# Performance work log

Measured on AMD Instinct MI355X. Metric: run time of the kernel, lower is better.

The kernel has to match this reference:

```python
import jax, jax.numpy as jnp
import numpy as np

N = 10000      # nodes
E = 160000     # directed edges (script symmetrizes; random here)
IN = 512       # input feature dim
H = 512        # hidden dim
OUT = 16       # classes


def setup_inputs() -> dict:
    key = jax.random.key(0)
    ks = jax.random.split(key, 8)
    x = jax.random.normal(ks[0], (N, IN), dtype=jnp.float32)
    edge_index = jax.random.randint(ks[1], (2, E), 0, N, dtype=jnp.int64)

    def glorot(k, shape):
        lim = np.sqrt(6.0 / (shape[0] + shape[1])).astype(np.float32)
        return jax.random.uniform(k, shape, dtype=jnp.float32, minval=-lim, maxval=lim)

    W1 = glorot(ks[2], (IN, H));  b1 = jnp.zeros((H,), jnp.float32)
    W2 = glorot(ks[3], (H, H));   b2 = jnp.zeros((H,), jnp.float32)
    Wl = glorot(ks[4], (H, OUT)); bl = jnp.zeros((OUT,), jnp.float32)
    return {"x": x, "edge_index": edge_index,
            "W1": W1, "b1": b1, "W2": W2, "b2": b2, "Wl": Wl, "bl": bl}


def gcn_conv(x, edge_index, W, b):
    """PyG GCNConv: D^{-1/2}(A+I)D^{-1/2} X W + b, unit edge weights."""
    n = x.shape[0]
    src, dst = edge_index[0], edge_index[1]
    h = x @ W                                   # [N, H] transform first (in<=out path)
    # degree with self-loops (all edge weights = 1)
    deg = jnp.zeros((n,), h.dtype).at[dst].add(1.0) + 1.0
    dinv = jax.lax.rsqrt(deg)                   # deg >= 1, no inf handling needed
    norm = dinv[src] * dinv[dst]                # [E]
    msgs = norm[:, None] * h[src]               # [E, H] gather + scale
    agg = jax.ops.segment_sum(msgs, dst, num_segments=n)
    agg = agg + (dinv * dinv)[:, None] * h      # self-loop contribution
    return agg + b


def reference(x, edge_index, W1, b1, W2, b2, Wl, bl):
    h = jax.nn.relu(gcn_conv(x, edge_index, W1, b1))
    # dropout is identity at inference
    h = jax.nn.relu(gcn_conv(h, edge_index, W2, b2))
    return h @ Wl + bl                          # [N, OUT] logits
```

## Files before the change

### kernel.cpp

```cpp
#include <hip/hip_runtime.h>
#include <stdint.h>

#define NF 512
#define OUT_F 16
#define PAD_DEG 128
#define GBM 64
#define GBN 128
#define GBK 32
#define NCHUNK 4

typedef __attribute__((ext_vector_type(8))) short short8v;
typedef __attribute__((ext_vector_type(4))) float f32x4;

#define GLOAD_LDS16(g, l) \
  __builtin_amdgcn_global_load_lds((const __attribute__((address_space(1))) unsigned int*)(g), \
                                   (__attribute__((address_space(3))) unsigned int*)(l), 16, 0, 0)


__device__ __forceinline__ void split2(float x, short& h, short& l) {
    unsigned u = __builtin_bit_cast(unsigned, x);
    unsigned hb = (u + 0x7fffu + ((u >> 16) & 1u)) & 0xffff0000u;
    h = (short)(hb >> 16);
    float r = x - __builtin_bit_cast(float, hb);
    unsigned v = __builtin_bit_cast(unsigned, r);
    unsigned lb = (v + 0x7fffu + ((v >> 16) & 1u)) & 0xffff0000u;
    l = (short)(lb >> 16);
}

__device__ __forceinline__ unsigned short bf16r(float x) {
    unsigned u = __builtin_bit_cast(unsigned, x);
    return (unsigned short)((u + 0x7fffu + ((u >> 16) & 1u)) >> 16);
}


__global__ void edge_prep_kernel(const int* __restrict__ src, const int* __restrict__ dst,
                                 int* __restrict__ counts, int* __restrict__ src_pad, int E) {
    int e = blockIdx.x * blockDim.x + threadIdx.x;
    if (e < E) {
        int d = dst[e];
        int slot = atomicAdd(&counts[d], 1);
        if (slot < PAD_DEG) src_pad[(size_t)d * PAD_DEG + slot] = src[e];
    }
}


__global__ __launch_bounds__(256) void convert_w_kernel(
    const float* __restrict__ W1, const float* __restrict__ W2,
    short* __restrict__ hi1, short* __restrict__ lo1,
    short* __restrict__ hi2, short* __restrict__ lo2) {
    __shared__ float tile[64][65];
    int id = blockIdx.x;
    const float* W;  short *WH, *WL;
    if (id < 64) { W = W1; WH = hi1; WL = lo1; }
    else         { W = W2; WH = hi2; WL = lo2; id -= 64; }
    int k0 = (id & 7) * 64, n0 = (id >> 3) * 64;
    int tr = threadIdx.x >> 4;
    int tc4 = (threadIdx.x & 15) * 4;
#pragma unroll
    for (int i = 0; i < 4; ++i) {
        int r = tr + i * 16;
        float4 v = *(const float4*)(W + (size_t)(k0 + r) * NF + n0 + tc4);
        tile[r][tc4 + 0] = v.x; tile[r][tc4 + 1] = v.y;
        tile[r][tc4 + 2] = v.z; tile[r][tc4 + 3] = v.w;
    }
    __syncthreads();
#pragma unroll
    for (int i = 0; i < 4; ++i) {
        int n = tr + i * 16;
        short h[4], l[4];
#pragma unroll
        for (int j = 0; j < 4; ++j) split2(tile[tc4 + j][n], h[j], l[j]);
        size_t off = (size_t)(n0 + n) * NF + k0 + tc4;
        *(short4*)(WH + off) = make_short4(h[0], h[1], h[2], h[3]);
        *(short4*)(WL + off) = make_short4(l[0], l[1], l[2], l[3]);
    }
}


__global__ __launch_bounds__(256) void convert_x_kernel(
    const float* __restrict__ x, short* __restrict__ xhi, short* __restrict__ xlo,
    int Nreal, int Mp) {
    int idx = blockIdx.x * 256 + threadIdx.x;
    int row = idx >> 7;
    int c4 = (idx & 127) * 4;
    if (row >= Mp) return;
    float4 v = make_float4(0.f, 0.f, 0.f, 0.f);
    if (row < Nreal) v = *(const float4*)(x + (size_t)row * NF + c4);
    short h[4], l[4];
    split2(v.x, h[0], l[0]); split2(v.y, h[1], l[1]);
    split2(v.z, h[2], l[2]); split2(v.w, h[3], l[3]);
    size_t off = (size_t)row * NF + c4;
    *(short4*)(xhi + off) = make_short4(h[0], h[1], h[2], h[3]);
    *(short4*)(xlo + off) = make_short4(l[0], l[1], l[2], l[3]);
}


__global__ __launch_bounds__(256) void gemm_mfma_kernel(
    const short* __restrict__ Ahi, const short* __restrict__ Alo,
    const short* __restrict__ BhiT, const short* __restrict__ BloT,
    const int* __restrict__ counts, unsigned short* __restrict__ Cb) {
    __shared__ short lds[2 * GBM * GBK + 2 * GBN * GBK];
    short* As_hi = lds;
    short* As_lo = lds + GBM * GBK;
    short* Bs_hi = lds + 2 * GBM * GBK;
    short* Bs_lo = lds + 2 * GBM * GBK + GBN * GBK;

    int t = threadIdx.x;
    int w = t >> 6, lane = t & 63, l15 = lane & 15, q = lane >> 4;
    int m0 = (blockIdx.x >> 2) * GBM;
    int n0 = (blockIdx.x & 3) * GBN;
    int wr = w >> 1, wc = w & 1;

    int gr = lane >> 2;
    int gk = (lane & 3) * 8;
    const short* Ahi_g = Ahi + (size_t)(m0 + w * 16 + gr) * NF + gk;
    const short* Alo_g = Alo + (size_t)(m0 + w * 16 + gr) * NF + gk;
    const short* Bhi_g0 = BhiT + (size_t)(n0 + w * 16 + gr) * NF + gk;
    const short* Bhi_g1 = BhiT + (size_t)(n0 + (w + 4) * 16 + gr) * NF + gk;
    const short* Blo_g0 = BloT + (size_t)(n0 + w * 16 + gr) * NF + gk;
    const short* Blo_g1 = BloT + (size_t)(n0 + (w + 4) * 16 + gr) * NF + gk;
    short* As_hi_d = As_hi + w * 16 * GBK;
    short* As_lo_d = As_lo + w * 16 * GBK;
    short* Bs_hi_d0 = Bs_hi + w * 16 * GBK;
    short* Bs_hi_d1 = Bs_hi + (w + 4) * 16 * GBK;
    short* Bs_lo_d0 = Bs_lo + w * 16 * GBK;
    short* Bs_lo_d1 = Bs_lo + (w + 4) * 16 * GBK;

    f32x4 acc[2][4] = {};

    for (int k0 = 0; k0 < NF; k0 += GBK) {
        GLOAD_LDS16(Ahi_g + k0, As_hi_d);
        GLOAD_LDS16(Alo_g + k0, As_lo_d);
        GLOAD_LDS16(Bhi_g0 + k0, Bs_hi_d0);
        GLOAD_LDS16(Bhi_g1 + k0, Bs_hi_d1);
        GLOAD_LDS16(Blo_g0 + k0, Bs_lo_d0);
        GLOAD_LDS16(Blo_g1 + k0, Bs_lo_d1);
        __syncthreads();

        short8v ahi[2], alo[2], bhi[4], blo[4];
#pragma unroll
        for (int r = 0; r < 2; ++r) {
            int off = (wr * 32 + r * 16 + l15) * GBK + q * 8;
            ahi[r] = *(const short8v*)(As_hi + off);
            alo[r] = *(const short8v*)(As_lo + off);
        }
#pragma unroll
        for (int c = 0; c < 4; ++c) {
            int off = (wc * 64 + c * 16 + l15) * GBK + q * 8;
            bhi[c] = *(const short8v*)(Bs_hi + off);
            blo[c] = *(const short8v*)(Bs_lo + off);
        }
#pragma unroll
        for (int r = 0; r < 2; ++r)
#pragma unroll
            for (int c = 0; c < 4; ++c) {
                acc[r][c] = __builtin_amdgcn_mfma_f32_16x16x32_bf16(ahi[r], bhi[c], acc[r][c], 0, 0, 0);
                acc[r][c] = __builtin_amdgcn_mfma_f32_16x16x32_bf16(ahi[r], blo[c], acc[r][c], 0, 0, 0);
                acc[r][c] = __builtin_amdgcn_mfma_f32_16x16x32_bf16(alo[r], bhi[c], acc[r][c], 0, 0, 0);
            }
        __syncthreads();
    }

#pragma unroll
    for (int r = 0; r < 2; ++r)
#pragma unroll
        for (int i = 0; i < 4; ++i) {
            int row = m0 + wr * 32 + r * 16 + q * 4 + i;
            float dv = rsqrtf((float)counts[row] + 1.0f);
#pragma unroll
            for (int c = 0; c < 4; ++c) {
                int col = n0 + wc * 64 + c * 16 + l15;
                Cb[(size_t)row * NF + col] = bf16r(acc[r][c][i] * dv);
            }
        }
}


__global__ __launch_bounds__(256) void agg_kernel(
    const unsigned short* __restrict__ hb, const int* __restrict__ counts,
    const int* __restrict__ src_pad, const float* __restrict__ bias,
    short* __restrict__ out_hi, short* __restrict__ out_lo,
    float* __restrict__ out32, int Mreal, int split_out) {
    int chunk = blockIdx.x & (NCHUNK - 1);
    int node = (blockIdx.x >> 2) * 4 + (threadIdx.x >> 6);
    int lane = threadIdx.x & 63;
    int g = lane >> 4;
    int j = lane & 15;
    int f8 = chunk * 128 + j * 8;
    size_t obase = (size_t)node * NF + f8;

    if (node >= Mreal) {
        if (g == 0) {
            if (split_out) {
                short8v z = {0, 0, 0, 0, 0, 0, 0, 0};
                *(short8v*)(out_hi + obase) = z;
                *(short8v*)(out_lo + obase) = z;
            } else {
                *(float4*)(out32 + obase) = make_float4(0.f, 0.f, 0.f, 0.f);
                *(float4*)(out32 + obase + 4) = make_float4(0.f, 0.f, 0.f, 0.f);
            }
        }
        return;
    }

    int cntr = counts[node];
    int cnt = cntr < PAD_DEG ? cntr : PAD_DEG;
    const int* sp = src_pad + (size_t)node * PAD_DEG;

    float acc[8] = {};
    for (int e = 0; e < cnt; e += 16) {
        int4 s4 = *(const int4*)(sp + e + g * 4);
        int base = e + g * 4;
        int sidx[4] = {s4.x, s4.y, s4.z, s4.w};
#pragma unroll
        for (int tq = 0; tq < 4; ++tq) {
            bool ok = (base + tq) < cnt;
            int srow = ok ? sidx[tq] : node;
            float m = ok ? 1.f : 0.f;
            uint4 pv = *(const uint4*)(hb + (size_t)srow * NF + f8);
            acc[0] = fmaf(m, __builtin_bit_cast(float, pv.x << 16), acc[0]);
            acc[1] = fmaf(m, __builtin_bit_cast(float, pv.x & 0xffff0000u), acc[1]);
            acc[2] = fmaf(m, __builtin_bit_cast(float, pv.y << 16), acc[2]);
            acc[3] = fmaf(m, __builtin_bit_cast(float, pv.y & 0xffff0000u), acc[3]);
            acc[4] = fmaf(m, __builtin_bit_cast(float, pv.z << 16), acc[4]);
            acc[5] = fmaf(m, __builtin_bit_cast(float, pv.z & 0xffff0000u), acc[5]);
            acc[6] = fmaf(m, __builtin_bit_cast(float, pv.w << 16), acc[6]);
            acc[7] = fmaf(m, __builtin_bit_cast(float, pv.w & 0xffff0000u), acc[7]);
        }
    }

#pragma unroll
    for (int k = 0; k < 8; ++k) {
        acc[k] += __shfl_xor(acc[k], 16);
        acc[k] += __shfl_xor(acc[k], 32);
    }

    if (g != 0) return;

    uint4 sv = *(const uint4*)(hb + obase);
    float self[8];
    self[0] = __builtin_bit_cast(float, sv.x << 16);
    self[1] = __builtin_bit_cast(float, sv.x & 0xffff0000u);
    self[2] = __builtin_bit_cast(float, sv.y << 16);
    self[3] = __builtin_bit_cast(float, sv.y & 0xffff0000u);
    self[4] = __builtin_bit_cast(float, sv.z << 16);
    self[5] = __builtin_bit_cast(float, sv.z & 0xffff0000u);
    self[6] = __builtin_bit_cast(float, sv.w << 16);
    self[7] = __builtin_bit_cast(float, sv.w & 0xffff0000u);

    float dv = rsqrtf((float)cntr + 1.0f);
    float o[8];
#pragma unroll
    for (int k = 0; k < 8; ++k)
        o[k] = fmaxf(fmaf(dv, acc[k] + self[k], bias[f8 + k]), 0.f);

    if (split_out) {
        short8v h8, l8;
#pragma unroll
        for (int k = 0; k < 8; ++k) { short hh, ll; split2(o[k], hh, ll); h8[k] = hh; l8[k] = ll; }
        *(short8v*)(out_hi + obase) = h8;
        *(short8v*)(out_lo + obase) = l8;
    } else {
        *(float4*)(out32 + obase) = make_float4(o[0], o[1], o[2], o[3]);
        *(float4*)(out32 + obase + 4) = make_float4(o[4], o[5], o[6], o[7]);
    }
}


__global__ __launch_bounds__(256) void head_kernel(
    const float* __restrict__ in, const float* __restrict__ Wl,
    const float* __restrict__ bl, float* __restrict__ out, int M) {
    __shared__ float Ws[NF * OUT_F];
    int tid = threadIdx.x;
    for (int i = tid; i < NF * OUT_F; i += 256) Ws[i] = Wl[i];
    __syncthreads();
    int node = blockIdx.x * 16 + (tid >> 4);
    int o = tid & 15;
    if (node >= M) return;
    const float4* row4 = (const float4*)(in + (size_t)node * NF);
    float acc = 0.f;
#pragma unroll 4
    for (int k4 = 0; k4 < NF / 4; ++k4) {
        float4 rv = row4[k4];
        int kb = k4 * 4;
        acc += rv.x * Ws[(kb + 0) * OUT_F + o] + rv.y * Ws[(kb + 1) * OUT_F + o]
             + rv.z * Ws[(kb + 2) * OUT_F + o] + rv.w * Ws[(kb + 3) * OUT_F + o];
    }
    out[(size_t)node * OUT_F + o] = acc + bl[o];
}


extern "C" void kernel_launch(void* const* d_in, const int* in_sizes, int n_in,
                              void* d_out, int out_size, void* d_ws, size_t ws_size,
                              hipStream_t stream) {
    const float* x  = (const float*)d_in[0];
    const int* eidx = (const int*)d_in[1];
    const float* W1 = (const float*)d_in[2];
    const float* b1 = (const float*)d_in[3];
    const float* W2 = (const float*)d_in[4];
    const float* b2 = (const float*)d_in[5];
    const float* Wl = (const float*)d_in[6];
    const float* bl = (const float*)d_in[7];

    int N = in_sizes[0] / NF;
    int E = in_sizes[1] / 2;
    int Mp = (N + GBM - 1) & ~(GBM - 1);
    const int* src = eidx;
    const int* dst = eidx + E;

    char* p = (char*)d_ws;
    auto carve = [&](size_t bytes) -> void* {
        void* r = (void*)p;
        p += (bytes + 255) & ~(size_t)255;
        return r;
    };
    unsigned short* hbuf = (unsigned short*)carve((size_t)Mp * NF * sizeof(unsigned short));
    short* splitbuf = (short*)carve((size_t)Mp * NF * 2 * sizeof(short));
    short* s_hi     = splitbuf;
    short* s_lo     = splitbuf + (size_t)Mp * NF;
    float* aggout   = (float*)splitbuf;
    short* W1hiT    = (short*)carve((size_t)NF * NF * sizeof(short));
    short* W1loT    = (short*)carve((size_t)NF * NF * sizeof(short));
    short* W2hiT    = (short*)carve((size_t)NF * NF * sizeof(short));
    short* W2loT    = (short*)carve((size_t)NF * NF * sizeof(short));
    int*   counts   = (int*)carve((size_t)Mp * sizeof(int));
    int*   src_pad  = (int*)carve((size_t)N * PAD_DEG * sizeof(int));

    hipMemsetAsync(counts, 0, (size_t)Mp * sizeof(int), stream);

    edge_prep_kernel<<<dim3((E + 255) / 256), dim3(256), 0, stream>>>(src, dst, counts, src_pad, E);
    convert_w_kernel<<<dim3(128), dim3(256), 0, stream>>>(W1, W2, W1hiT, W1loT, W2hiT, W2loT);
    convert_x_kernel<<<dim3(Mp * (NF / 4) / 256), dim3(256), 0, stream>>>(x, s_hi, s_lo, N, Mp);

    dim3 gg((Mp / GBM) * (NF / GBN));
    dim3 ga(Mp);

    gemm_mfma_kernel<<<gg, dim3(256), 0, stream>>>(s_hi, s_lo, W1hiT, W1loT, counts, hbuf);
    agg_kernel<<<ga, dim3(256), 0, stream>>>(hbuf, counts, src_pad, b1,
                                             s_hi, s_lo, (float*)nullptr, N, 1);
    gemm_mfma_kernel<<<gg, dim3(256), 0, stream>>>(s_hi, s_lo, W2hiT, W2loT, counts, hbuf);
    agg_kernel<<<ga, dim3(256), 0, stream>>>(hbuf, counts, src_pad, b2,
                                             (short*)nullptr, (short*)nullptr, aggout, N, 0);
    head_kernel<<<dim3((N + 15) / 16), dim3(256), 0, stream>>>(aggout, Wl, bl, (float*)d_out, N);
}
```

Before: 205.4 us.

## Switch pipeline from split-bf16 to single fp16 operands with swizzled LDS GEMM

Replaces the three-pass hi/lo bf16 split GEMM with a single fp16 MFMA pass, and stores all intermediates (inputs, messages, aggregated activations) in fp16 instead of split bf16 or fp32. The GEMM K-tile grows to 64 with an XOR-swizzled LDS layout to avoid bank conflicts. This cuts MFMA work to a third and halves the conversion, aggregation and head memory traffic. In exchange it loses the near-fp32 accuracy of the split scheme and relies on fp16 range and precision being enough for the tolerance.

```diff
diff --git a/kernel.cpp b/kernel.cpp
--- a/kernel.cpp
+++ b/kernel.cpp
@@ -6,31 +6,15 @@
 #define PAD_DEG 128
 #define GBM 64
 #define GBN 128
-#define GBK 32
 #define NCHUNK 4
 
-typedef __attribute__((ext_vector_type(8))) short short8v;
+typedef __attribute__((ext_vector_type(8))) _Float16 half8;
+typedef __attribute__((ext_vector_type(4))) _Float16 half4v;
 typedef __attribute__((ext_vector_type(4))) float f32x4;
 
 #define GLOAD_LDS16(g, l) \
   __builtin_amdgcn_global_load_lds((const __attribute__((address_space(1))) unsigned int*)(g), \
                                    (__attribute__((address_space(3))) unsigned int*)(l), 16, 0, 0)
-
-
-__device__ __forceinline__ void split2(float x, short& h, short& l) {
-    unsigned u = __builtin_bit_cast(unsigned, x);
-    unsigned hb = (u + 0x7fffu + ((u >> 16) & 1u)) & 0xffff0000u;
-    h = (short)(hb >> 16);
-    float r = x - __builtin_bit_cast(float, hb);
-    unsigned v = __builtin_bit_cast(unsigned, r);
-    unsigned lb = (v + 0x7fffu + ((v >> 16) & 1u)) & 0xffff0000u;
-    l = (short)(lb >> 16);
-}
-
-__device__ __forceinline__ unsigned short bf16r(float x) {
-    unsigned u = __builtin_bit_cast(unsigned, x);
-    return (unsigned short)((u + 0x7fffu + ((u >> 16) & 1u)) >> 16);
-}
 
 
 __global__ void edge_prep_kernel(const int* __restrict__ src, const int* __restrict__ dst,
@@ -46,13 +30,12 @@
 
 __global__ __launch_bounds__(256) void convert_w_kernel(
     const float* __restrict__ W1, const float* __restrict__ W2,
-    short* __restrict__ hi1, short* __restrict__ lo1,
-    short* __restrict__ hi2, short* __restrict__ lo2) {
+    _Float16* __restrict__ T1, _Float16* __restrict__ T2) {
     __shared__ float tile[64][65];
     int id = blockIdx.x;
-    const float* W;  short *WH, *WL;
-    if (id < 64) { W = W1; WH = hi1; WL = lo1; }
-    else         { W = W2; WH = hi2; WL = lo2; id -= 64; }
+    const float* W;  _Float16* WT;
+    if (id < 64) { W = W1; WT = T1; }
+    else         { W = W2; WT = T2; id -= 64; }
     int k0 = (id & 7) * 64, n0 = (id >> 3) * 64;
     int tr = threadIdx.x >> 4;
     int tc4 = (threadIdx.x & 15) * 4;
@@ -67,43 +50,39 @@
 #pragma unroll
     for (int i = 0; i < 4; ++i) {
         int n = tr + i * 16;
-        short h[4], l[4];
-#pragma unroll
-        for (int j = 0; j < 4; ++j) split2(tile[tc4 + j][n], h[j], l[j]);
-        size_t off = (size_t)(n0 + n) * NF + k0 + tc4;
-        *(short4*)(WH + off) = make_short4(h[0], h[1], h[2], h[3]);
-        *(short4*)(WL + off) = make_short4(l[0], l[1], l[2], l[3]);
+        half4v hv;
+#pragma unroll
+        for (int j = 0; j < 4; ++j) hv[j] = (_Float16)tile[tc4 + j][n];
+        *(half4v*)(WT + (size_t)(n0 + n) * NF + k0 + tc4) = hv;
     }
 }
 
 
 __global__ __launch_bounds__(256) void convert_x_kernel(
-    const float* __restrict__ x, short* __restrict__ xhi, short* __restrict__ xlo,
-    int Nreal, int Mp) {
+    const float* __restrict__ x, _Float16* __restrict__ x16, int Nreal, int Mp) {
     int idx = blockIdx.x * 256 + threadIdx.x;
-    int row = idx >> 7;
-    int c4 = (idx & 127) * 4;
+    int row = idx >> 6;
+    int c8 = (idx & 63) * 8;
     if (row >= Mp) return;
-    float4 v = make_float4(0.f, 0.f, 0.f, 0.f);
-    if (row < Nreal) v = *(const float4*)(x + (size_t)row * NF + c4);
-    short h[4], l[4];
-    split2(v.x, h[0], l[0]); split2(v.y, h[1], l[1]);
-    split2(v.z, h[2], l[2]); split2(v.w, h[3], l[3]);
-    size_t off = (size_t)row * NF + c4;
-    *(short4*)(xhi + off) = make_short4(h[0], h[1], h[2], h[3]);
-    *(short4*)(xlo + off) = make_short4(l[0], l[1], l[2], l[3]);
+    half8 hv = {0, 0, 0, 0, 0, 0, 0, 0};
+    if (row < Nreal) {
+        float4 v0 = *(const float4*)(x + (size_t)row * NF + c8);
+        float4 v1 = *(const float4*)(x + (size_t)row * NF + c8 + 4);
+        hv[0] = (_Float16)v0.x; hv[1] = (_Float16)v0.y;
+        hv[2] = (_Float16)v0.z; hv[3] = (_Float16)v0.w;
+        hv[4] = (_Float16)v1.x; hv[5] = (_Float16)v1.y;
+        hv[6] = (_Float16)v1.z; hv[7] = (_Float16)v1.w;
+    }
+    *(half8*)(x16 + (size_t)row * NF + c8) = hv;
 }
 
 
 __global__ __launch_bounds__(256) void gemm_mfma_kernel(
-    const short* __restrict__ Ahi, const short* __restrict__ Alo,
-    const short* __restrict__ BhiT, const short* __restrict__ BloT,
-    const int* __restrict__ counts, unsigned short* __restrict__ Cb) {
-    __shared__ short lds[2 * GBM * GBK + 2 * GBN * GBK];
-    short* As_hi = lds;
-    short* As_lo = lds + GBM * GBK;
-    short* Bs_hi = lds + 2 * GBM * GBK;
-    short* Bs_lo = lds + 2 * GBM * GBK + GBN * GBK;
+    const _Float16* __restrict__ A, const _Float16* __restrict__ BT,
+    const int* __restrict__ counts, _Float16* __restrict__ Ch) {
+    __shared__ _Float16 lds[GBM * 64 + GBN * 64];
+    _Float16* As = lds;
+    _Float16* Bs = lds + GBM * 64;
 
     int t = threadIdx.x;
     int w = t >> 6, lane = t & 63, l15 = lane & 15, q = lane >> 4;
@@ -111,53 +90,49 @@
     int n0 = (blockIdx.x & 3) * GBN;
     int wr = w >> 1, wc = w & 1;
 
-    int gr = lane >> 2;
-    int gk = (lane & 3) * 8;
-    const short* Ahi_g = Ahi + (size_t)(m0 + w * 16 + gr) * NF + gk;
-    const short* Alo_g = Alo + (size_t)(m0 + w * 16 + gr) * NF + gk;
-    const short* Bhi_g0 = BhiT + (size_t)(n0 + w * 16 + gr) * NF + gk;
-    const short* Bhi_g1 = BhiT + (size_t)(n0 + (w + 4) * 16 + gr) * NF + gk;
-    const short* Blo_g0 = BloT + (size_t)(n0 + w * 16 + gr) * NF + gk;
-    const short* Blo_g1 = BloT + (size_t)(n0 + (w + 4) * 16 + gr) * NF + gk;
-    short* As_hi_d = As_hi + w * 16 * GBK;
-    short* As_lo_d = As_lo + w * 16 * GBK;
-    short* Bs_hi_d0 = Bs_hi + w * 16 * GBK;
-    short* Bs_hi_d1 = Bs_hi + (w + 4) * 16 * GBK;
-    short* Bs_lo_d0 = Bs_lo + w * 16 * GBK;
-    short* Bs_lo_d1 = Bs_lo + (w + 4) * 16 * GBK;
+    int gr = lane >> 3;
+    int gc = ((lane & 7) ^ (gr & 7)) * 8;
+    const _Float16* Ag0 = A + (size_t)(m0 + w * 8 + gr) * NF + gc;
+    const _Float16* Ag1 = A + (size_t)(m0 + 32 + w * 8 + gr) * NF + gc;
+    const _Float16* Bg0 = BT + (size_t)(n0 + w * 8 + gr) * NF + gc;
+    const _Float16* Bg1 = BT + (size_t)(n0 + 32 + w * 8 + gr) * NF + gc;
+    const _Float16* Bg2 = BT + (size_t)(n0 + 64 + w * 8 + gr) * NF + gc;
+    const _Float16* Bg3 = BT + (size_t)(n0 + 96 + w * 8 + gr) * NF + gc;
+    _Float16* As_d0 = As + (w * 8) * 64;
+    _Float16* As_d1 = As + (32 + w * 8) * 64;
+    _Float16* Bs_d0 = Bs + (w * 8) * 64;
+    _Float16* Bs_d1 = Bs + (32 + w * 8) * 64;
+    _Float16* Bs_d2 = Bs + (64 + w * 8) * 64;
+    _Float16* Bs_d3 = Bs + (96 + w * 8) * 64;
 
     f32x4 acc[2][4] = {};
 
-    for (int k0 = 0; k0 < NF; k0 += GBK) {
-        GLOAD_LDS16(Ahi_g + k0, As_hi_d);
-        GLOAD_LDS16(Alo_g + k0, As_lo_d);
-        GLOAD_LDS16(Bhi_g0 + k0, Bs_hi_d0);
-        GLOAD_LDS16(Bhi_g1 + k0, Bs_hi_d1);
-        GLOAD_LDS16(Blo_g0 + k0, Bs_lo_d0);
-        GLOAD_LDS16(Blo_g1 + k0, Bs_lo_d1);
+    for (int k0 = 0; k0 < NF; k0 += 64) {
+        GLOAD_LDS16(Ag0 + k0, As_d0);
+        GLOAD_LDS16(Ag1 + k0, As_d1);
+        GLOAD_LDS16(Bg0 + k0, Bs_d0);
+        GLOAD_LDS16(Bg1 + k0, Bs_d1);
+        GLOAD_LDS16(Bg2 + k0, Bs_d2);
+        GLOAD_LDS16(Bg3 + k0, Bs_d3);
         __syncthreads();
 
-        short8v ahi[2], alo[2], bhi[4], blo[4];
-#pragma unroll
-        for (int r = 0; r < 2; ++r) {
-            int off = (wr * 32 + r * 16 + l15) * GBK + q * 8;
-            ahi[r] = *(const short8v*)(As_hi + off);
-            alo[r] = *(const short8v*)(As_lo + off);
-        }
-#pragma unroll
-        for (int c = 0; c < 4; ++c) {
-            int off = (wc * 64 + c * 16 + l15) * GBK + q * 8;
-            bhi[c] = *(const short8v*)(Bs_hi + off);
-            blo[c] = *(const short8v*)(Bs_lo + off);
-        }
-#pragma unroll
-        for (int r = 0; r < 2; ++r)
-#pragma unroll
-            for (int c = 0; c < 4; ++c) {
-                acc[r][c] = __builtin_amdgcn_mfma_f32_16x16x32_bf16(ahi[r], bhi[c], acc[r][c], 0, 0, 0);
-                acc[r][c] = __builtin_amdgcn_mfma_f32_16x16x32_bf16(ahi[r], blo[c], acc[r][c], 0, 0, 0);
-                acc[r][c] = __builtin_amdgcn_mfma_f32_16x16x32_bf16(alo[r], bhi[c], acc[r][c], 0, 0, 0);
-            }
+        int key = l15 & 7;
+#pragma unroll
+        for (int kk = 0; kk < 2; ++kk) {
+            int ch = ((kk * 4 + q) ^ key) * 8;
+            half8 a[2], b[4];
+#pragma unroll
+            for (int r = 0; r < 2; ++r)
+                a[r] = *(const half8*)(As + (wr * 32 + r * 16 + l15) * 64 + ch);
+#pragma unroll
+            for (int c = 0; c < 4; ++c)
+                b[c] = *(const half8*)(Bs + (wc * 64 + c * 16 + l15) * 64 + ch);
+#pragma unroll
+            for (int r = 0; r < 2; ++r)
+#pragma unroll
+                for (int c = 0; c < 4; ++c)
+                    acc[r][c] = __builtin_amdgcn_mfma_f32_16x16x32_f16(a[r], b[c], acc[r][c], 0, 0, 0);
+        }
         __syncthreads();
     }
 
@@ -170,17 +145,16 @@
 #pragma unroll
             for (int c = 0; c < 4; ++c) {
                 int col = n0 + wc * 64 + c * 16 + l15;
-                Cb[(size_t)row * NF + col] = bf16r(acc[r][c][i] * dv);
+                Ch[(size_t)row * NF + col] = (_Float16)(acc[r][c][i] * dv);
             }
         }
 }
 
 
 __global__ __launch_bounds__(256) void agg_kernel(
-    const unsigned short* __restrict__ hb, const int* __restrict__ counts,
+    const _Float16* __restrict__ hb, const int* __restrict__ counts,
     const int* __restrict__ src_pad, const float* __restrict__ bias,
-    short* __restrict__ out_hi, short* __restrict__ out_lo,
-    float* __restrict__ out32, int Mreal, int split_out) {
+    _Float16* __restrict__ out_h, int Mreal) {
     int chunk = blockIdx.x & (NCHUNK - 1);
     int node = (blockIdx.x >> 2) * 4 + (threadIdx.x >> 6);
     int lane = threadIdx.x & 63;
@@ -191,14 +165,8 @@
 
     if (node >= Mreal) {
         if (g == 0) {
-            if (split_out) {
-                short8v z = {0, 0, 0, 0, 0, 0, 0, 0};
-                *(short8v*)(out_hi + obase) = z;
-                *(short8v*)(out_lo + obase) = z;
-            } else {
-                *(float4*)(out32 + obase) = make_float4(0.f, 0.f, 0.f, 0.f);
-                *(float4*)(out32 + obase + 4) = make_float4(0.f, 0.f, 0.f, 0.f);
-            }
+            half8 z = {0, 0, 0, 0, 0, 0, 0, 0};
+            *(half8*)(out_h + obase) = z;
         }
         return;
     }
@@ -217,15 +185,9 @@
             bool ok = (base + tq) < cnt;
             int srow = ok ? sidx[tq] : node;
             float m = ok ? 1.f : 0.f;
-            uint4 pv = *(const uint4*)(hb + (size_t)srow * NF + f8);
-            acc[0] = fmaf(m, __builtin_bit_cast(float, pv.x << 16), acc[0]);
-            acc[1] = fmaf(m, __builtin_bit_cast(float, pv.x & 0xffff0000u), acc[1]);
-            acc[2] = fmaf(m, __builtin_bit_cast(float, pv.y << 16), acc[2]);
-            acc[3] = fmaf(m, __builtin_bit_cast(float, pv.y & 0xffff0000u), acc[3]);
-            acc[4] = fmaf(m, __builtin_bit_cast(float, pv.z << 16), acc[4]);
-            acc[5] = fmaf(m, __builtin_bit_cast(float, pv.z & 0xffff0000u), acc[5]);
-            acc[6] = fmaf(m, __builtin_bit_cast(float, pv.w << 16), acc[6]);
-            acc[7] = fmaf(m, __builtin_bit_cast(float, pv.w & 0xffff0000u), acc[7]);
+            half8 hv = *(const half8*)(hb + (size_t)srow * NF + f8);
+#pragma unroll
+            for (int k = 0; k < 8; ++k) acc[k] = fmaf(m, (float)hv[k], acc[k]);
         }
     }
 
@@ -237,38 +199,20 @@
 
     if (g != 0) return;
 
-    uint4 sv = *(const uint4*)(hb + obase);
-    float self[8];
-    self[0] = __builtin_bit_cast(float, sv.x << 16);
-    self[1] = __builtin_bit_cast(float, sv.x & 0xffff0000u);
-    self[2] = __builtin_bit_cast(float, sv.y << 16);
-    self[3] = __builtin_bit_cast(float, sv.y & 0xffff0000u);
-    self[4] = __builtin_bit_cast(float, sv.z << 16);
-    self[5] = __builtin_bit_cast(float, sv.z & 0xffff0000u);
-    self[6] = __builtin_bit_cast(float, sv.w << 16);
-    self[7] = __builtin_bit_cast(float, sv.w & 0xffff0000u);
-
+    half8 sv = *(const half8*)(hb + obase);
     float dv = rsqrtf((float)cntr + 1.0f);
-    float o[8];
-#pragma unroll
-    for (int k = 0; k < 8; ++k)
-        o[k] = fmaxf(fmaf(dv, acc[k] + self[k], bias[f8 + k]), 0.f);
-
-    if (split_out) {
-        short8v h8, l8;
-#pragma unroll
-        for (int k = 0; k < 8; ++k) { short hh, ll; split2(o[k], hh, ll); h8[k] = hh; l8[k] = ll; }
-        *(short8v*)(out_hi + obase) = h8;
-        *(short8v*)(out_lo + obase) = l8;
-    } else {
-        *(float4*)(out32 + obase) = make_float4(o[0], o[1], o[2], o[3]);
-        *(float4*)(out32 + obase + 4) = make_float4(o[4], o[5], o[6], o[7]);
-    }
+    half8 o8;
+#pragma unroll
+    for (int k = 0; k < 8; ++k) {
+        float o = fmaxf(fmaf(dv, acc[k] + (float)sv[k], bias[f8 + k]), 0.f);
+        o8[k] = (_Float16)o;
+    }
+    *(half8*)(out_h + obase) = o8;
 }
 
 
 __global__ __launch_bounds__(256) void head_kernel(
-    const float* __restrict__ in, const float* __restrict__ Wl,
+    const _Float16* __restrict__ in, const float* __restrict__ Wl,
     const float* __restrict__ bl, float* __restrict__ out, int M) {
     __shared__ float Ws[NF * OUT_F];
     int tid = threadIdx.x;
@@ -277,14 +221,15 @@
     int node = blockIdx.x * 16 + (tid >> 4);
     int o = tid & 15;
     if (node >= M) return;
-    const float4* row4 = (const float4*)(in + (size_t)node * NF);
+    const half8* row8 = (const half8*)(in + (size_t)node * NF);
     float acc = 0.f;
-#pragma unroll 4
-    for (int k4 = 0; k4 < NF / 4; ++k4) {
-        float4 rv = row4[k4];
-        int kb = k4 * 4;
-        acc += rv.x * Ws[(kb + 0) * OUT_F + o] + rv.y * Ws[(kb + 1) * OUT_F + o]
-             + rv.z * Ws[(kb + 2) * OUT_F + o] + rv.w * Ws[(kb + 3) * OUT_F + o];
+#pragma unroll 2
+    for (int k8 = 0; k8 < NF / 8; ++k8) {
+        half8 hv = row8[k8];
+        int kb = k8 * 8;
+#pragma unroll
+        for (int u = 0; u < 8; ++u)
+            acc = fmaf((float)hv[u], Ws[(kb + u) * OUT_F + o], acc);
     }
     out[(size_t)node * OUT_F + o] = acc + bl[o];
 }
@@ -314,32 +259,25 @@
         p += (bytes + 255) & ~(size_t)255;
         return r;
     };
-    unsigned short* hbuf = (unsigned short*)carve((size_t)Mp * NF * sizeof(unsigned short));
-    short* splitbuf = (short*)carve((size_t)Mp * NF * 2 * sizeof(short));
-    short* s_hi     = splitbuf;
-    short* s_lo     = splitbuf + (size_t)Mp * NF;
-    float* aggout   = (float*)splitbuf;
-    short* W1hiT    = (short*)carve((size_t)NF * NF * sizeof(short));
-    short* W1loT    = (short*)carve((size_t)NF * NF * sizeof(short));
-    short* W2hiT    = (short*)carve((size_t)NF * NF * sizeof(short));
-    short* W2loT    = (short*)carve((size_t)NF * NF * sizeof(short));
-    int*   counts   = (int*)carve((size_t)Mp * sizeof(int));
-    int*   src_pad  = (int*)carve((size_t)N * PAD_DEG * sizeof(int));
+    _Float16* hbuf = (_Float16*)carve((size_t)Mp * NF * sizeof(_Float16));
+    _Float16* abuf = (_Float16*)carve((size_t)Mp * NF * sizeof(_Float16));
+    _Float16* W1T  = (_Float16*)carve((size_t)NF * NF * sizeof(_Float16));
+    _Float16* W2T  = (_Float16*)carve((size_t)NF * NF * sizeof(_Float16));
+    int* counts    = (int*)carve((size_t)Mp * sizeof(int));
+    int* src_pad   = (int*)carve((size_t)N * PAD_DEG * sizeof(int));
 
     hipMemsetAsync(counts, 0, (size_t)Mp * sizeof(int), stream);
 
     edge_prep_kernel<<<dim3((E + 255) / 256), dim3(256), 0, stream>>>(src, dst, counts, src_pad, E);
-    convert_w_kernel<<<dim3(128), dim3(256), 0, stream>>>(W1, W2, W1hiT, W1loT, W2hiT, W2loT);
-    convert_x_kernel<<<dim3(Mp * (NF / 4) / 256), dim3(256), 0, stream>>>(x, s_hi, s_lo, N, Mp);
+    convert_w_kernel<<<dim3(128), dim3(256), 0, stream>>>(W1, W2, W1T, W2T);
+    convert_x_kernel<<<dim3(Mp / 4), dim3(256), 0, stream>>>(x, abuf, N, Mp);
 
     dim3 gg((Mp / GBM) * (NF / GBN));
     dim3 ga(Mp);
 
-    gemm_mfma_kernel<<<gg, dim3(256), 0, stream>>>(s_hi, s_lo, W1hiT, W1loT, counts, hbuf);
-    agg_kernel<<<ga, dim3(256), 0, stream>>>(hbuf, counts, src_pad, b1,
-                                             s_hi, s_lo, (float*)nullptr, N, 1);
-    gemm_mfma_kernel<<<gg, dim3(256), 0, stream>>>(s_hi, s_lo, W2hiT, W2loT, counts, hbuf);
-    agg_kernel<<<ga, dim3(256), 0, stream>>>(hbuf, counts, src_pad, b2,
-                                             (short*)nullptr, (short*)nullptr, aggout, N, 0);
-    head_kernel<<<dim3((N + 15) / 16), dim3(256), 0, stream>>>(aggout, Wl, bl, (float*)d_out, N);
-}
+    gemm_mfma_kernel<<<gg, dim3(256), 0, stream>>>(abuf, W1T, counts, hbuf);
+    agg_kernel<<<ga, dim3(256), 0, stream>>>(hbuf, counts, src_pad, b1, abuf, N);
+    gemm_mfma_kernel<<<gg, dim3(256), 0, stream>>>(abuf, W2T, counts, hbuf);
+    agg_kernel<<<ga, dim3(256), 0, stream>>>(hbuf, counts, src_pad, b2, abuf, N);
+    head_kernel<<<dim3((N + 15) / 16), dim3(256), 0, stream>>>(abuf, Wl, bl, (float*)d_out, N);
+}
```

Result: faster. 172.6 us (-16.0%).
